# Optimization experiments

Measured on AMD Instinct MI355X. Metric: run time of the kernel, lower is better.

## Reference

```python
import jax, jax.numpy as jnp
import numpy as np

B = 128        # graphs per batch
N = 512        # nodes per graph (equal-size graphs -> dense mask all True)
F_IN = 128     # dataset.num_features
HID = 128      # hidden
C3 = 3 * HID   # num_layers * hidden (pool in_channels)
HEADS = 5
NC = 2         # num_classes
KC = NC + 1    # num_clusters2 = num_clusters_per_class*(num_classes+1) = 3
NC1 = NC       # num_clusters1 = num_clusters_per_class*num_classes = 2
OUT = 16       # pool out_channels
EPER = 8192    # edges per graph
TAU = 1.0
L1, L2 = 10.0, 0.01
BN_EPS = 1e-5


def setup_inputs() -> dict:
    key = jax.random.key(0)
    ks = jax.random.split(key, 12)
    Nn = B * N
    E = B * EPER
    x = jax.random.normal(ks[0], (Nn, F_IN), jnp.float32)
    local = jax.random.randint(ks[1], (2, E), 0, N)
    off = (jnp.repeat(jnp.arange(B), EPER) * N)[None, :]
    edge_index = (local + off).astype(jnp.int64)  # global node ids, per-graph blocks
    y = jax.random.randint(ks[2], (B,), 0, NC).astype(jnp.int64)

    def w(k_, shp, fan):
        return (jax.random.normal(k_, shp, jnp.float32) / np.sqrt(fan)).astype(jnp.float32)

    params = dict(
        W1=w(ks[3], (F_IN, HID), F_IN), b1=jnp.zeros((HID,), jnp.float32),
        W2=w(ks[4], (HID, HID), HID), b2=jnp.zeros((HID,), jnp.float32),
        W3=w(ks[5], (HID, HID), HID), b3=jnp.zeros((HID,), jnp.float32),
        bn_gamma=jnp.ones((C3,), jnp.float32), bn_beta=jnp.zeros((C3,), jnp.float32),
        k=w(ks[6], (HEADS, KC, C3), C3),
        lin_pool_W=w(ks[7], (C3, OUT), C3),
        lin1_W=w(ks[8], (NC1 * OUT, HID), NC1 * OUT), lin1_b=jnp.zeros((HID,), jnp.float32),
        lin2_W=w(ks[9], (HID, NC), HID), lin2_b=jnp.zeros((NC,), jnp.float32),
    )
    return dict(x=x, edge_index=edge_index, y=y, **params)


def reference(x, edge_index, y, W1, b1, W2, b2, W3, b3, bn_gamma, bn_beta, k,
              lin_pool_W, lin1_W, lin1_b, lin2_W, lin2_b):
    src, dst = edge_index[0], edge_index[1]
    Nn = x.shape[0]

    # GCNConv (normalize=False): out[dst] += (h @ W)[src] ; + bias
    def gcn(h, W, b):
        m = h @ W
        return jnp.zeros_like(m).at[dst].add(m[src]) + b

    h1 = jax.nn.relu(gcn(x, W1, b1))
    h2 = jax.nn.relu(gcn(h1, W2, b2))
    h3 = jax.nn.relu(gcn(h2, W3, b3))
    X = jnp.concatenate([h1, h2, h3], axis=1)  # [Nn, C3]

    # BatchNorm1d (training-mode batch stats, biased var)
    mu = X.mean(0)
    var = X.var(0)
    Xn = (X - mu) / jnp.sqrt(var + BN_EPS) * bn_gamma + bn_beta

    # --- IMPO pool ---
    H, K, C = k.shape
    k2 = k.reshape(H * K, C)
    # squared euclidean cdist: [H*K, Nn]
    d2 = jnp.maximum((k2 ** 2).sum(-1)[:, None] + (Xn ** 2).sum(-1)[None, :]
                     - 2.0 * (k2 @ Xn.T), 0.0)
    dist = (1.0 + d2 / TAU) ** (-(TAU + 1.0) / 2.0)
    dist = dist.reshape(H, K, B, N).transpose(2, 0, 3, 1)  # [B,H,N,K]
    Sh = dist / dist.sum(-1, keepdims=True)
    S = Sh.sum(1)  # sum over heads -> [B,N,K]; mask is all-True

    # per-graph adjacency aggregation: out[row] += S[col], then degree norm
    Sf = S.reshape(Nn, K)
    Sagg = jnp.zeros_like(Sf).at[src].add(Sf[dst])
    deg = (jnp.zeros((Nn,), Sf.dtype).at[src].add(1.0).at[dst].add(1.0)) / 2.0
    deg = jnp.where(deg == 0, 1.0, deg)
    S_raw = (Sagg / deg[:, None]).reshape(B, N, K)

    # use_gumbel=False path: softmax + hard argmax mask
    g = jax.nn.softmax(S_raw, axis=-1)
    onehot = jax.nn.one_hot(jnp.argmax(g, -1), K, dtype=g.dtype)
    Sfin = g * onehot

    xd = Xn.reshape(B, N, C)
    xp = jnp.einsum('bnk,bnc->bkc', Sfin, xd) @ lin_pool_W  # [B,K,OUT]
    out_x = xp[:, :NC1, :]

    # --- impo_loss ---
    yb = jnp.broadcast_to(y[:, None], (B, N))
    assigned = jnp.argmax(Sfin, -1)
    ac = assigned  # cluster_map is identity for num_clusters_per_class=1
    mr = (ac < NC) & (ac == yb)
    mw = (ac < NC) & (ac != yb)
    sum_loss = Sfin.sum(1)[:, :NC1].sum(1).mean()
    mf = (mr | mw).astype(Sfin.dtype)
    counts = jnp.zeros((NC,), Sfin.dtype).at[yb.reshape(-1)].add(mf.reshape(-1))
    bc = jnp.ones((NC,), Sfin.dtype) + counts
    weight = bc.max() / (bc + 0.001)
    logits = Sfin[..., :KC - 1]  # drop last cluster column
    logp = jax.nn.log_softmax(logits, axis=-1)
    ce = -jnp.take_along_axis(logp, yb[..., None], axis=-1)[..., 0]
    wsamp = weight[yb] * mf
    cel = (wsamp * ce).sum() / jnp.maximum(wsamp.sum(), 1e-12)
    total_loss = L1 * cel + L2 * sum_loss

    # head
    xf = out_x.reshape(B, -1)
    xf = jax.nn.relu(xf @ lin1_W + lin1_b)
    out = jax.nn.log_softmax(xf @ lin2_W + lin2_b, axis=-1)
    return (out, total_loss)
```

## Files before the change

### kernel.cpp

```cpp
#include <hip/hip_runtime.h>
#include <hip/hip_bf16.h>

#define BB 128
#define NV 512
#define NN (BB*NV)
#define EPER_C 8192
#define E_TOT (BB*EPER_C)
#define BN_EPS_F 1e-5f

typedef unsigned int u32;
typedef unsigned short u16;

__device__ __forceinline__ float bfu2f_lo(u32 w) { return __uint_as_float(w << 16); }
__device__ __forceinline__ float bfu2f_hi(u32 w) { return __uint_as_float(w & 0xFFFF0000u); }
__device__ __forceinline__ u16 f2bf(float f) {
    u32 u = __float_as_uint(f);
    u32 r = (u + 0x7FFFu + ((u >> 16) & 1u)) >> 16;
    return (u16)r;
}
__device__ __forceinline__ u32 pack2(float a, float b) {
    return (u32)f2bf(a) | ((u32)f2bf(b) << 16);
}
__device__ __forceinline__ float f16u2f(u16 h) {
    const u32 s = ((u32)h & 0x8000u) << 16;
    const u32 e = (h >> 10) & 0x1Fu;
    const u32 m = h & 0x3FFu;
    if (e == 0u) {
        float v = (float)m * 5.9604644775390625e-8f;
        return s ? -v : v;
    }
    if (e == 31u) return __uint_as_float(s | 0x7F800000u | (m << 13));
    return __uint_as_float(s | ((e + 112u) << 23) | (m << 13));
}
__device__ __forceinline__ float san(float v) {
    if (!(v == v)) return 0.f;
    return fminf(fmaxf(v, -1e30f), 1e30f);
}

__device__ __forceinline__ float2 h_ld2(const u32* H, size_t i2, int hf32) {
    float2 v;
    if (hf32) {
        v = ((const float2*)H)[i2];
    } else {
        const u32 w = H[i2];
        v.x = bfu2f_lo(w);
        v.y = bfu2f_hi(w);
    }
    return v;
}
__device__ __forceinline__ void h_st2(u32* H, size_t i2, float a, float b, int hf32) {
    if (hf32) {
        float2 v;
        v.x = a;
        v.y = b;
        ((float2*)H)[i2] = v;
    } else {
        H[i2] = pack2(a, b);
    }
}
__device__ __forceinline__ float h_ld1(const u32* H, size_t i, int hf32) {
    if (hf32) return ((const float*)H)[i];
    return __uint_as_float(((u32)((const u16*)H)[i]) << 16);
}

__global__ void fill_out_kernel(float* o, float v) {
    int i = blockIdx.x * 256 + threadIdx.x;
    if (i < 257) o[i] = v;
}

__global__ void init_kernel(u32* p, int n) {
    int i = blockIdx.x * 256 + threadIdx.x;
    if (i < n) p[i] = 0u;
}

__global__ void probe_kernel(const u32* g, const u32* e, u32* flags) {
    const int t = threadIdx.x;
    u32 acc = 0u;
    for (int i = t; i < 2048; i += 64) acc |= e[2 * i + 1];
#pragma unroll
    for (int s = 32; s > 0; s >>= 1) acc |= (u32)__shfl_xor((int)acc, s);
    if (t == 0) {
        const u32 w = g[0];
        u32 cls = 0u;
        if (w == 0x3F800000u) cls = 1u;
        else if (w == 0x3C003C00u) cls = 2u;
        flags[9] = cls;
        flags[8] = (acc != 0u) ? 1u : 0u;
    }
}

__device__ __forceinline__ int ld_src(const int* e, int is64, size_t i) {
    return (is64 ? e[2 * i] : e[i]) & (NN - 1);
}
__device__ __forceinline__ int ld_dst(const int* e, int is64, size_t i) {
    return (is64 ? e[2 * ((size_t)E_TOT + i)] : e[(size_t)E_TOT + i]) & (NN - 1);
}
__device__ __forceinline__ int ld_y(const int* y, int is64, int bi) {
    return (is64 ? y[2 * bi] : y[bi]) & 1;
}

#define CVT_TOT 66690
struct CvtPtrs { const void* p[14]; };
__global__ __launch_bounds__(256) void cvt_all_kernel(CvtPtrs ptrs, float* __restrict__ dst,
                                                      const u32* __restrict__ flags) {
    const int i = blockIdx.x * 256 + threadIdx.x;
    if (i >= CVT_TOT) return;
    const int kPof[14] = {0, 16384, 16512, 32896, 33024, 49408, 49536, 49920,
                          50304, 56064, 62208, 66304, 66432, 66688};
    const void* pp = ptrs.p[0];
    int base = 0;
#pragma unroll
    for (int s2 = 1; s2 < 14; ++s2) {
        if (i >= kPof[s2]) { pp = ptrs.p[s2]; base = kPof[s2]; }
    }
    const int off = i - base;
    const u32 cls = flags[9];
    float v;
    if (cls == 1u) v = ((const float*)pp)[off];
    else if (cls == 2u) v = f16u2f(((const u16*)pp)[off]);
    else v = __uint_as_float(((u32)((const u16*)pp)[off]) << 16);
    dst[i] = v;
}

__global__ __launch_bounds__(256) void csr_kernel(const int* __restrict__ eidx,
                                                  const u32* __restrict__ flags,
                                                  u16* __restrict__ sortedD,
                                                  u32* __restrict__ rpD) {
    __shared__ u32 cntD[512];
    __shared__ u32 offD[512];
    __shared__ u32 p[256];
    const int bi = blockIdx.x;
    const int t = threadIdx.x;
    const int is64 = (flags[8] == 0u);
    for (int i = t; i < 512; i += 256) cntD[i] = 0u;
    __syncthreads();
    const size_t eb = (size_t)bi * EPER_C;
    for (int e = t; e < EPER_C; e += 256) {
        const int dl = ld_dst(eidx, is64, eb + e) & 511;
        atomicAdd(&cntD[dl], 1u);
    }
    __syncthreads();
    const u32 a0 = cntD[2 * t], a1 = cntD[2 * t + 1];
    p[t] = a0 + a1;
    __syncthreads();
    for (int d = 1; d < 256; d <<= 1) {
        u32 va = p[t];
        if (t >= d) va += p[t - d];
        __syncthreads();
        p[t] = va;
        __syncthreads();
    }
    {
        const u32 exD = p[t] - (a0 + a1);
        offD[2 * t] = exD;
        offD[2 * t + 1] = exD + a0;
    }
    __syncthreads();
    for (int i = t; i < 512; i += 256) rpD[bi * 513 + i] = offD[i];
    if (t == 0) rpD[bi * 513 + 512] = EPER_C;
    for (int i = t; i < 512; i += 256) cntD[i] = 0u;
    __syncthreads();
    for (int e = t; e < EPER_C; e += 256) {
        const int sl = ld_src(eidx, is64, eb + e) & 511;
        const int dl = ld_dst(eidx, is64, eb + e) & 511;
        const u32 pos = offD[dl] + atomicAdd(&cntD[dl], 1u);
        sortedD[eb + pos] = (u16)sl;
    }
}

__global__ __launch_bounds__(1024, 4) void gemm_k(const u32* __restrict__ X2,
                                                  const float* __restrict__ Wc,
                                                  u32* __restrict__ Y2,
                                                  const u32* __restrict__ flags,
                                                  int xmode, int hf32) {
    __shared__ float xsT[128][132];
    __shared__ float ws[128][128];
    const int n0 = blockIdx.x * 128;
    const int t = threadIdx.x;
    const int tx = t & 31, ty = t >> 5;
    u32 cls;
    if (xmode) cls = flags[9];
    else cls = hf32 ? 1u : 0u;

    if (cls == 1u) {
        const float4* Xf4 = (const float4*)X2;
#pragma unroll
        for (int i = 0; i < 2; ++i) {
            const int idx = t + i * 1024;
            const int r = idx >> 4, q = idx & 15;
            const float4 v = Xf4[(size_t)(n0 + r) * 32 + q];
            xsT[4 * q + 0][r] = v.x;
            xsT[4 * q + 1][r] = v.y;
            xsT[4 * q + 2][r] = v.z;
            xsT[4 * q + 3][r] = v.w;
        }
    } else if (cls == 2u) {
#pragma unroll
        for (int i = 0; i < 4; ++i) {
            const int idx = t + i * 1024;
            const int r = idx >> 5, wq = idx & 31;
            const u32 w = X2[(size_t)(n0 + r) * 64 + wq];
            xsT[2 * wq + 0][r] = f16u2f((u16)(w & 0xFFFFu));
            xsT[2 * wq + 1][r] = f16u2f((u16)(w >> 16));
        }
    } else {
#pragma unroll
        for (int i = 0; i < 4; ++i) {
            const int idx = t + i * 1024;
            const int r = idx >> 5, wq = idx & 31;
            const u32 w = X2[(size_t)(n0 + r) * 64 + wq];
            xsT[2 * wq + 0][r] = bfu2f_lo(w);
            xsT[2 * wq + 1][r] = bfu2f_hi(w);
        }
    }
    {
        const float4* Wf4 = (const float4*)Wc;
#pragma unroll
        for (int i = 0; i < 2; ++i) {
            const int idx = t + i * 1024;
            const int kr = idx >> 5, cq = idx & 31;
            *(float4*)&ws[kr][4 * cq] = Wf4[(size_t)kr * 32 + cq];
        }
    }
    __syncthreads();

    float4 px0, px1, pw0, pw1;
    u32 pxu0 = 0, pxu1 = 0, pxu2 = 0, pxu3 = 0;
    if (cls == 1u) {
        const float4* Xf4 = (const float4*)X2;
        {
            const int r = t >> 4, q = t & 15;
            px0 = Xf4[(size_t)(n0 + r) * 32 + 16 + q];
        }
        {
            const int idx = t + 1024;
            const int r = idx >> 4, q = idx & 15;
            px1 = Xf4[(size_t)(n0 + r) * 32 + 16 + q];
        }
    } else {
        const int r0 = t >> 5, wq = t & 31;
        pxu0 = X2[(size_t)(n0 + r0) * 64 + 32 + wq];
        pxu1 = X2[(size_t)(n0 + r0 + 32) * 64 + 32 + wq];
        pxu2 = X2[(size_t)(n0 + r0 + 64) * 64 + 32 + wq];
        pxu3 = X2[(size_t)(n0 + r0 + 96) * 64 + 32 + wq];
    }
    {
        const float4* Wf4 = (const float4*)Wc;
        pw0 = Wf4[(size_t)(64 + (t >> 5)) * 32 + (t & 31)];
        pw1 = Wf4[(size_t)(96 + (t >> 5)) * 32 + (t & 31)];
    }

    float a[4][4];
#pragma unroll
    for (int r = 0; r < 4; ++r)
#pragma unroll
        for (int c = 0; c < 4; ++c) a[r][c] = 0.f;

#pragma unroll 4
    for (int k = 0; k < 64; ++k) {
        const float4 xv = *(const float4*)&xsT[k][4 * ty];
        const float4 wv = *(const float4*)&ws[k][4 * tx];
        a[0][0] += xv.x * wv.x; a[0][1] += xv.x * wv.y; a[0][2] += xv.x * wv.z; a[0][3] += xv.x * wv.w;
        a[1][0] += xv.y * wv.x; a[1][1] += xv.y * wv.y; a[1][2] += xv.y * wv.z; a[1][3] += xv.y * wv.w;
        a[2][0] += xv.z * wv.x; a[2][1] += xv.z * wv.y; a[2][2] += xv.z * wv.z; a[2][3] += xv.z * wv.w;
        a[3][0] += xv.w * wv.x; a[3][1] += xv.w * wv.y; a[3][2] += xv.w * wv.z; a[3][3] += xv.w * wv.w;
    }

    if (cls == 1u) {
        {
            const int r = t >> 4, q = t & 15;
            xsT[64 + 4 * q + 0][r] = px0.x;
            xsT[64 + 4 * q + 1][r] = px0.y;
            xsT[64 + 4 * q + 2][r] = px0.z;
            xsT[64 + 4 * q + 3][r] = px0.w;
        }
        {
            const int idx = t + 1024;
            const int r = idx >> 4, q = idx & 15;
            xsT[64 + 4 * q + 0][r] = px1.x;
            xsT[64 + 4 * q + 1][r] = px1.y;
            xsT[64 + 4 * q + 2][r] = px1.z;
            xsT[64 + 4 * q + 3][r] = px1.w;
        }
    } else if (cls == 2u) {
        const int r0 = t >> 5, wq = t & 31;
        xsT[64 + 2 * wq + 0][r0] = f16u2f((u16)(pxu0 & 0xFFFFu));
        xsT[64 + 2 * wq + 1][r0] = f16u2f((u16)(pxu0 >> 16));
        xsT[64 + 2 * wq + 0][r0 + 32] = f16u2f((u16)(pxu1 & 0xFFFFu));
        xsT[64 + 2 * wq + 1][r0 + 32] = f16u2f((u16)(pxu1 >> 16));
        xsT[64 + 2 * wq + 0][r0 + 64] = f16u2f((u16)(pxu2 & 0xFFFFu));
        xsT[64 + 2 * wq + 1][r0 + 64] = f16u2f((u16)(pxu2 >> 16));
        xsT[64 + 2 * wq + 0][r0 + 96] = f16u2f((u16)(pxu3 & 0xFFFFu));
        xsT[64 + 2 * wq + 1][r0 + 96] = f16u2f((u16)(pxu3 >> 16));
    } else {
        const int r0 = t >> 5, wq = t & 31;
        xsT[64 + 2 * wq + 0][r0] = bfu2f_lo(pxu0);
        xsT[64 + 2 * wq + 1][r0] = bfu2f_hi(pxu0);
        xsT[64 + 2 * wq + 0][r0 + 32] = bfu2f_lo(pxu1);
        xsT[64 + 2 * wq + 1][r0 + 32] = bfu2f_hi(pxu1);
        xsT[64 + 2 * wq + 0][r0 + 64] = bfu2f_lo(pxu2);
        xsT[64 + 2 * wq + 1][r0 + 64] = bfu2f_hi(pxu2);
        xsT[64 + 2 * wq + 0][r0 + 96] = bfu2f_lo(pxu3);
        xsT[64 + 2 * wq + 1][r0 + 96] = bfu2f_hi(pxu3);
    }
    {
        *(float4*)&ws[64 + (t >> 5)][4 * (t & 31)] = pw0;
        *(float4*)&ws[96 + (t >> 5)][4 * (t & 31)] = pw1;
    }
    __syncthreads();

#pragma unroll 4
    for (int k = 64; k < 128; ++k) {
        const float4 xv = *(const float4*)&xsT[k][4 * ty];
        const float4 wv = *(const float4*)&ws[k][4 * tx];
        a[0][0] += xv.x * wv.x; a[0][1] += xv.x * wv.y; a[0][2] += xv.x * wv.z; a[0][3] += xv.x * wv.w;
        a[1][0] += xv.y * wv.x; a[1][1] += xv.y * wv.y; a[1][2] += xv.y * wv.z; a[1][3] += xv.y * wv.w;
        a[2][0] += xv.z * wv.x; a[2][1] += xv.z * wv.y; a[2][2] += xv.z * wv.z; a[2][3] += xv.z * wv.w;
        a[3][0] += xv.w * wv.x; a[3][1] += xv.w * wv.y; a[3][2] += xv.w * wv.z; a[3][3] += xv.w * wv.w;
    }

#pragma unroll
    for (int r = 0; r < 4; ++r) {
        const size_t n = (size_t)n0 + 4 * ty + r;
        if (hf32) {
            float4 o;
            o.x = a[r][0]; o.y = a[r][1]; o.z = a[r][2]; o.w = a[r][3];
            ((float4*)Y2)[n * 32 + tx] = o;
        } else {
            Y2[n * 64 + 2 * tx + 0] = pack2(a[r][0], a[r][1]);
            Y2[n * 64 + 2 * tx + 1] = pack2(a[r][2], a[r][3]);
        }
    }
}

__global__ __launch_bounds__(1024) void gcn_lds_k(const u16* __restrict__ sortedD,
                                                  const u32* __restrict__ rpD,
                                                  const float* __restrict__ bias,
                                                  u32* __restrict__ M2,
                                                  float* __restrict__ bnacc,
                                                  int col_base, int hf32) {
    __shared__ float Ms[512 * 64];
    __shared__ u32 srt32[EPER_C / 2];
    __shared__ u32 rp[513];
    const int t = threadIdx.x;
    const int bi = blockIdx.x >> 1;
    const int hf = blockIdx.x & 1;
    const size_t rowbase = (size_t)bi * 512;
    const u16* srt = (const u16*)srt32;

    const u32* srcw = (const u32*)(sortedD + (size_t)bi * EPER_C);
    for (int i = t; i < EPER_C / 2; i += 1024) srt32[i] = srcw[i];
    for (int i = t; i < 513; i += 1024) rp[i] = rpD[bi * 513 + i];

    if (hf32) {
        const float4* src4 = (const float4*)M2;
        float4* dst4 = (float4*)Ms;
        for (int idx = t; idx < 512 * 16; idx += 1024) {
            const int r = idx >> 4, q = idx & 15;
            dst4[r * 16 + q] = src4[(rowbase + r) * 32 + hf * 16 + q];
        }
    } else {
        for (int idx = t; idx < 512 * 32; idx += 1024) {
            const int r = idx >> 5, q = idx & 31;
            const u32 w = M2[(rowbase + r) * 64 + hf * 32 + q];
            Ms[r * 64 + 2 * q] = bfu2f_lo(w);
            Ms[r * 64 + 2 * q + 1] = bfu2f_hi(w);
        }
    }
    __syncthreads();

    const int j = t & 15;
    const int g = t >> 4;
    const float4* M4 = (const float4*)Ms;
    const float bx = bias[hf * 64 + j * 4 + 0];
    const float by = bias[hf * 64 + j * 4 + 1];
    const float bz = bias[hf * 64 + j * 4 + 2];
    const float bw = bias[hf * 64 + j * 4 + 3];
    float S0 = 0.f, S1 = 0.f, S2 = 0.f, S3 = 0.f;
    float Q0 = 0.f, Q1 = 0.f, Q2 = 0.f, Q3 = 0.f;

#pragma unroll
    for (int gi = 0; gi < 8; ++gi) {
        const int l = g + gi * 64;
        u32 r1 = rp[l + 1];
        if (r1 > EPER_C) r1 = EPER_C;
        u32 r0 = rp[l];
        if (r0 > r1) r0 = r1;
        float ax = 0.f, ay = 0.f, az = 0.f, aw = 0.f;
        u32 idx = r0;
        for (; idx + 4 <= r1; idx += 4) {
            const int sa = srt[idx];
            const int sb = srt[idx + 1];
            const int sc = srt[idx + 2];
            const int sd = srt[idx + 3];
            const float4 va = M4[sa * 16 + j];
            const float4 vb = M4[sb * 16 + j];
            const float4 vc = M4[sc * 16 + j];
            const float4 vd = M4[sd * 16 + j];
            ax += va.x + vb.x; ay += va.y + vb.y; az += va.z + vb.z; aw += va.w + vb.w;
            ax += vc.x + vd.x; ay += vc.y + vd.y; az += vc.z + vd.z; aw += vc.w + vd.w;
        }
        for (; idx < r1; ++idx) {
            const int sa = srt[idx];
            const float4 va = M4[sa * 16 + j];
            ax += va.x; ay += va.y; az += va.z; aw += va.w;
        }
        float vx = san(ax + bx); vx = vx > 0.f ? vx : 0.f;
        float vy = san(ay + by); vy = vy > 0.f ? vy : 0.f;
        float vz = san(az + bz); vz = vz > 0.f ? vz : 0.f;
        float vw = san(aw + bw); vw = vw > 0.f ? vw : 0.f;
        if (hf32) {
            float4 o; o.x = vx; o.y = vy; o.z = vz; o.w = vw;
            ((float4*)M2)[(rowbase + l) * 32 + hf * 16 + j] = o;
        } else {
            const size_t pr = (rowbase + l) * 64 + hf * 32 + 2 * j;
            M2[pr] = pack2(vx, vy);
            M2[pr + 1] = pack2(vz, vw);
        }
        S0 += vx; S1 += vy; S2 += vz; S3 += vw;
        Q0 += vx * vx; Q1 += vy * vy; Q2 += vz * vz; Q3 += vw * vw;
    }

    S0 += __shfl_xor(S0, 16); Q0 += __shfl_xor(Q0, 16);
    S1 += __shfl_xor(S1, 16); Q1 += __shfl_xor(Q1, 16);
    S2 += __shfl_xor(S2, 16); Q2 += __shfl_xor(Q2, 16);
    S3 += __shfl_xor(S3, 16); Q3 += __shfl_xor(Q3, 16);
    S0 += __shfl_xor(S0, 32); Q0 += __shfl_xor(Q0, 32);
    S1 += __shfl_xor(S1, 32); Q1 += __shfl_xor(Q1, 32);
    S2 += __shfl_xor(S2, 32); Q2 += __shfl_xor(Q2, 32);
    S3 += __shfl_xor(S3, 32); Q3 += __shfl_xor(Q3, 32);

    __syncthreads();
    float* red = (float*)srt32;
    const int lane = t & 63;
    const int wid = t >> 6;
    if (lane < 16) {
        float* rw = &red[(wid * 16 + j) * 8];
        rw[0] = S0; rw[1] = Q0; rw[2] = S1; rw[3] = Q1;
        rw[4] = S2; rw[5] = Q2; rw[6] = S3; rw[7] = Q3;
    }
    __syncthreads();
    if (t < 128) {
        float s = 0.f;
        for (int w = 0; w < 16; ++w) s += red[w * 128 + t];
        const int jj = t >> 3;
        const int cc = (t >> 1) & 3;
        const int st = t & 1;
        atomicAdd(&bnacc[(size_t)(col_base + hf * 64 + jj * 4 + cc) * 2 + st], s);
    }
}

__global__ __launch_bounds__(384) void bn2_kernel(const float* __restrict__ bnacc,
                                                  const float* __restrict__ gamma,
                                                  const float* __restrict__ beta,
                                                  float* __restrict__ scaleA,
                                                  float* __restrict__ shiftA) {
    const int c = threadIdx.x;
    const float s = bnacc[c * 2 + 0];
    const float s2 = bnacc[c * 2 + 1];
    const float inv_n = 1.f / (float)NN;
    const float mu = san(s * inv_n);
    float var = san(s2 * inv_n - mu * mu);
    var = var > 0.f ? var : 0.f;
    const float sc = san(gamma[c] / sqrtf(var + BN_EPS_F));
    scaleA[c] = sc;
    shiftA[c] = san(beta[c] - mu * sc);
}

__global__ __launch_bounds__(256) void dist_kernel(const u32* __restrict__ h1,
                                                   const u32* __restrict__ h2,
                                                   const u32* __restrict__ h3,
                                                   const float* __restrict__ kc,
                                                   const float* __restrict__ scaleA,
                                                   const float* __restrict__ shiftA,
                                                   float4* __restrict__ Sf4, int hf32) {
    __shared__ float k2f[15 * 384];
    __shared__ float scl[384], shf[384];
    __shared__ float ksq[15];
    const int t = threadIdx.x;
    for (int i = t; i < 15 * 384; i += 256) k2f[i] = kc[i];
    for (int i = t; i < 384; i += 256) {
        scl[i] = scaleA[i];
        shf[i] = shiftA[i];
    }
    __syncthreads();
    if (t < 15) {
        float q = 0.f;
        for (int c2 = 0; c2 < 384; ++c2) {
            const float v = k2f[t * 384 + c2];
            q += v * v;
        }
        ksq[t] = q;
    }
    __syncthreads();
    const int n = blockIdx.x * 128 + (t >> 1);
    const int sub = t & 1;
    float acc[15];
#pragma unroll
    for (int j = 0; j < 15; ++j) acc[j] = 0.f;
    float xq = 0.f;
#pragma unroll
    for (int pL = 0; pL < 3; ++pL) {
        const u32* hp = (pL == 0) ? h1 : (pL == 1) ? h2 : h3;
        for (int q8 = sub; q8 < 16; q8 += 2) {
            float xv[8];
            if (hf32) {
                const float4 va = ((const float4*)hp)[(size_t)n * 32 + q8 * 2 + 0];
                const float4 vb = ((const float4*)hp)[(size_t)n * 32 + q8 * 2 + 1];
                xv[0] = va.x; xv[1] = va.y; xv[2] = va.z; xv[3] = va.w;
                xv[4] = vb.x; xv[5] = vb.y; xv[6] = vb.z; xv[7] = vb.w;
            } else {
                const uint4 w = ((const uint4*)hp)[(size_t)n * 16 + q8];
                xv[0] = bfu2f_lo(w.x); xv[1] = bfu2f_hi(w.x);
                xv[2] = bfu2f_lo(w.y); xv[3] = bfu2f_hi(w.y);
                xv[4] = bfu2f_lo(w.z); xv[5] = bfu2f_hi(w.z);
                xv[6] = bfu2f_lo(w.w); xv[7] = bfu2f_hi(w.w);
            }
            const int c = pL * 128 + q8 * 8;
#pragma unroll
            for (int i = 0; i < 8; ++i) {
                const float x = xv[i] * scl[c + i] + shf[c + i];
                xv[i] = x;
                xq += x * x;
            }
#pragma unroll
            for (int j = 0; j < 15; ++j) {
                const float* kr = &k2f[j * 384 + c];
                float a = acc[j];
#pragma unroll
                for (int i = 0; i < 8; ++i) a += xv[i] * kr[i];
                acc[j] = a;
            }
        }
    }
#pragma unroll
    for (int j = 0; j < 15; ++j) acc[j] += __shfl_xor(acc[j], 1);
    xq += __shfl_xor(xq, 1);
    if (sub == 0) {
        float dist[15];
#pragma unroll
        for (int j = 0; j < 15; ++j) {
            float d2 = san(ksq[j] + xq - 2.f * acc[j]);
            d2 = d2 > 0.f ? d2 : 0.f;
            dist[j] = 1.f / (1.f + d2);
        }
        float S0 = 0.f, S1 = 0.f, S2 = 0.f;
#pragma unroll
        for (int h = 0; h < 5; ++h) {
            const float a = dist[h * 3 + 0], b = dist[h * 3 + 1], cd = dist[h * 3 + 2];
            const float inv = 1.f / fmaxf(a + b + cd, 1e-30f);
            S0 += a * inv;
            S1 += b * inv;
            S2 += cd * inv;
        }
        float4 o;
        o.x = san(S0); o.y = san(S1); o.z = san(S2); o.w = 0.f;
        Sf4[n] = o;
    }
}

__global__ __launch_bounds__(256) void sagg_kernel(const int* __restrict__ eidx,
                                                   const u32* __restrict__ flags,
                                                   const float4* __restrict__ Sf4,
                                                   const int* __restrict__ y,
                                                   int* __restrict__ nodeK,
                                                   float* __restrict__ nodeW,
                                                   float* __restrict__ scal) {
    __shared__ float sacc[512 * 3];
    __shared__ unsigned int degc[512];
    __shared__ float rA[256], rB[256];
    const int bi = blockIdx.x;
    const int t = threadIdx.x;
    const int is64 = (flags[8] == 0u);
    for (int i = t; i < 512 * 3; i += 256) sacc[i] = 0.f;
    for (int i = t; i < 512; i += 256) degc[i] = 0u;
    __syncthreads();
    const size_t eb = (size_t)bi * EPER_C;
    for (int e = t; e < EPER_C; e += 256) {
        const int sg = ld_src(eidx, is64, eb + e);
        const int dg = ld_dst(eidx, is64, eb + e);
        const int sl = sg & 511;
        const int dl = dg & 511;
        const float4 sv = Sf4[dg];
        atomicAdd(&sacc[sl * 3 + 0], sv.x);
        atomicAdd(&sacc[sl * 3 + 1], sv.y);
        atomicAdd(&sacc[sl * 3 + 2], sv.z);
        atomicAdd(&degc[sl], 1u);
        atomicAdd(&degc[dl], 1u);
    }
    __syncthreads();
    float mfAcc = 0.f, slAcc = 0.f;
    for (int l = t; l < 512; l += 256) {
        const float cnt = (float)degc[l];
        const float degf = cnt > 0.f ? cnt * 0.5f : 1.f;
        const float inv = 1.f / degf;
        const float r0 = san(sacc[l * 3 + 0] * inv);
        const float r1 = san(sacc[l * 3 + 1] * inv);
        const float r2 = san(sacc[l * 3 + 2] * inv);
        int am = 0;
        float mx = r0;
        if (r1 > mx) { mx = r1; am = 1; }
        if (r2 > mx) { mx = r2; am = 2; }
        const float e0 = expf(r0 - mx), e1 = expf(r1 - mx), e2 = expf(r2 - mx);
        const float g = san(1.f / (e0 + e1 + e2));
        const int n = bi * 512 + l;
        nodeK[n] = am;
        nodeW[n] = g;
        if (am < 2) {
            mfAcc += 1.f;
            slAcc += g;
        }
    }
    rA[t] = mfAcc;
    rB[t] = slAcc;
    __syncthreads();
    for (int sft = 128; sft > 0; sft >>= 1) {
        if (t < sft) {
            rA[t] += rA[t + sft];
            rB[t] += rB[t + sft];
        }
        __syncthreads();
    }
    if (t == 0) {
        atomicAdd(&scal[ld_y(y, is64, bi)], rA[0]);
        atomicAdd(&scal[2], rB[0]);
    }
}

__global__ __launch_bounds__(256) void ce_kernel(const int* __restrict__ nodeK,
                                                 const float* __restrict__ nodeW,
                                                 const u32* __restrict__ flags,
                                                 const int* __restrict__ y,
                                                 float* __restrict__ scal) {
    const int n = blockIdx.x * 256 + threadIdx.x;
    const int bi = n >> 9;
    const int is64 = (flags[8] == 0u);
    const int kn = nodeK[n];
    float wce = 0.f, wsum = 0.f;
    if (kn >= 0 && kn < 2) {
        const float w = nodeW[n];
        const int yb = ld_y(y, is64, bi);
        const float l0 = (kn == 0) ? w : 0.f;
        const float l1 = (kn == 1) ? w : 0.f;
        const float m = fmaxf(l0, l1);
        const float lz = m + logf(expf(l0 - m) + expf(l1 - m));
        const float ce = lz - ((yb == 0) ? l0 : l1);
        const float bc0 = 1.f + scal[0];
        const float bc1 = 1.f + scal[1];
        const float bmax = fmaxf(bc0, bc1);
        const float wt = bmax / (((yb == 0) ? bc0 : bc1) + 0.001f);
        wce = san(wt * ce);
        wsum = san(wt);
    }
    __shared__ float rA[256], rB[256];
    const int t = threadIdx.x;
    rA[t] = wce;
    rB[t] = wsum;
    __syncthreads();
    for (int sft = 128; sft > 0; sft >>= 1) {
        if (t < sft) {
            rA[t] += rA[t + sft];
            rB[t] += rB[t + sft];
        }
        __syncthreads();
    }
    if (t == 0) {
        atomicAdd(&scal[3], rA[0]);
        atomicAdd(&scal[4], rB[0]);
    }
}

__global__ __launch_bounds__(384) void xp_kernel(const u32* __restrict__ h1,
                                                 const u32* __restrict__ h2,
                                                 const u32* __restrict__ h3,
                                                 const float* __restrict__ scaleA,
                                                 const float* __restrict__ shiftA,
                                                 const int* __restrict__ nodeK,
                                                 const float* __restrict__ nodeW,
                                                 float* __restrict__ xp, int hf32) {
    const int bi = blockIdx.x >> 2;
    const int ch = blockIdx.x & 3;
    const int c = threadIdx.x;
    const u32* harr = (c < 128) ? h1 : (c < 256) ? h2 : h3;
    const int cc = c & 127;
    const float sc = scaleA[c], sh = shiftA[c];
    float a0 = 0.f, a1 = 0.f;
    const int nb = bi * 512 + ch * 128;
    for (int l = 0; l < 128; ++l) {
        const int kn = nodeK[nb + l];
        if (kn >= 0 && kn < 2) {
            const float w = nodeW[nb + l];
            const float xv = h_ld1(harr, (size_t)(nb + l) * 128 + cc, hf32) * sc + sh;
            if (kn == 0) a0 += w * xv; else a1 += w * xv;
        }
    }
    atomicAdd(&xp[((size_t)bi * 2 + 0) * 384 + c], san(a0));
    atomicAdd(&xp[((size_t)bi * 2 + 1) * 384 + c], san(a1));
}

__global__ __launch_bounds__(128) void head_kernel(const float* __restrict__ xp,
                                                   const float* __restrict__ lpW,
                                                   const float* __restrict__ l1W,
                                                   const float* __restrict__ l1b,
                                                   const float* __restrict__ l2W,
                                                   const float* __restrict__ l2b,
                                                   float* __restrict__ outp) {
    const int bi = blockIdx.x;
    const int t = threadIdx.x;
    __shared__ float xfl[32];
    __shared__ float hidl[128];
    if (t < 32) {
        const int kk = t >> 4, o = t & 15;
        const float* xr = xp + ((size_t)bi * 2 + kk) * 384;
        float acc = 0.f;
        for (int c2 = 0; c2 < 384; ++c2) acc += xr[c2] * lpW[c2 * 16 + o];
        xfl[t] = san(acc);
    }
    __syncthreads();
    float acc = l1b[t];
    for (int i = 0; i < 32; ++i) acc += xfl[i] * l1W[i * 128 + t];
    hidl[t] = fmaxf(san(acc), 0.f);
    __syncthreads();
    if (t == 0) {
        float L0 = l2b[0], L1v = l2b[1];
        for (int j = 0; j < 128; ++j) {
            const float h = hidl[j];
            L0 += h * l2W[j * 2 + 0];
            L1v += h * l2W[j * 2 + 1];
        }
        L0 = san(L0); L1v = san(L1v);
        const float m = fmaxf(L0, L1v);
        const float ls = m + logf(expf(L0 - m) + expf(L1v - m));
        outp[bi * 2 + 0] = san(L0 - ls);
        outp[bi * 2 + 1] = san(L1v - ls);
    }
}

__global__ void fin_kernel(const float* __restrict__ scal, float* __restrict__ outp) {
    const float cel = san(scal[3] / fmaxf(scal[4], 1e-12f));
    const float total = san(10.f * cel + 0.01f * (scal[2] / (float)BB));
    outp[BB * 2] = total;
}

extern "C" void kernel_launch(void* const* d_in, const int* in_sizes, int n_in,
                              void* d_out, int out_size, void* d_ws, size_t ws_size,
                              hipStream_t stream) {
    (void)in_sizes; (void)n_in; (void)out_size;
    float* outp = (float*)d_out;

    const size_t tailW = (size_t)NN * 4 + (size_t)NN + (size_t)NN + 98304 + 16 + 768 + 768
                       + 66690 + 128 * 513 + (size_t)E_TOT / 2;
    const size_t needF = 3ull * NN * 128ull * 4ull + tailW * 4ull;
    const size_t needB = 3ull * NN * 128ull * 2ull + tailW * 4ull;
    int hf32;
    if (ws_size >= needF) hf32 = 1;
    else if (ws_size >= needB) hf32 = 0;
    else {
        fill_out_kernel<<<2, 256, 0, stream>>>(outp, 2000.f + (float)(ws_size >> 20));
        return;
    }

    const u32* xw = (const u32*)d_in[0];
    const int* eidx = (const int*)d_in[1];
    const int* y = (const int*)d_in[2];

    const size_t esz = hf32 ? 4u : 2u;
    char* base = (char*)d_ws;
    u32* H1 = (u32*)base;
    u32* H2 = (u32*)(base + (size_t)NN * 128 * esz);
    u32* H3 = (u32*)(base + 2 * (size_t)NN * 128 * esz);
    float* fb = (float*)(base + 3 * (size_t)NN * 128 * esz);
    float4* Sf4 = (float4*)fb;
    float* nodeW = fb + (size_t)NN * 4;
    int* nodeK = (int*)(nodeW + NN);
    float* xp = (float*)(nodeK + NN);
    float* scal = xp + 98304;
    u32* flags = (u32*)scal;
    float* bnacc = scal + 16;
    float* scaleA = bnacc + 768;
    float* shiftA = scaleA + 384;
    float* canon = shiftA + 384;
    u32* rpD = (u32*)(canon + 66690);
    u16* sortedD = (u16*)(rpD + 128 * 513);

    init_kernel<<<388, 256, 0, stream>>>((u32*)xp, 98304 + 16 + 768);
    probe_kernel<<<1, 64, 0, stream>>>((const u32*)d_in[9], (const u32*)eidx, flags);
    csr_kernel<<<BB, 256, 0, stream>>>(eidx, flags, sortedD, rpD);

    CvtPtrs cp;
    for (int i = 0; i < 14; ++i) cp.p[i] = d_in[3 + i];
    cvt_all_kernel<<<(CVT_TOT + 255) / 256, 256, 0, stream>>>(cp, canon, flags);

    gemm_k<<<NN / 128, 1024, 0, stream>>>(xw, canon + 0, H1, flags, 1, hf32);
    gcn_lds_k<<<BB * 2, 1024, 0, stream>>>(sortedD, rpD, canon + 16384, H1, bnacc, 0, hf32);
    gemm_k<<<NN / 128, 1024, 0, stream>>>(H1, canon + 16512, H2, flags, 0, hf32);
    gcn_lds_k<<<BB * 2, 1024, 0, stream>>>(sortedD, rpD, canon + 32896, H2, bnacc, 128, hf32);
    gemm_k<<<NN / 128, 1024, 0, stream>>>(H2, canon + 33024, H3, flags, 0, hf32);
    gcn_lds_k<<<BB * 2, 1024, 0, stream>>>(sortedD, rpD, canon + 49408, H3, bnacc, 256, hf32);
    bn2_kernel<<<1, 384, 0, stream>>>(bnacc, canon + 49536, canon + 49920, scaleA, shiftA);
    dist_kernel<<<NN / 128, 256, 0, stream>>>(H1, H2, H3, canon + 50304, scaleA, shiftA,
                                              Sf4, hf32);
    sagg_kernel<<<BB, 256, 0, stream>>>(eidx, flags, Sf4, y, nodeK, nodeW, scal);
    ce_kernel<<<NN / 256, 256, 0, stream>>>(nodeK, nodeW, flags, y, scal);
    xp_kernel<<<BB * 4, 384, 0, stream>>>(H1, H2, H3, scaleA, shiftA, nodeK, nodeW, xp, hf32);
    head_kernel<<<BB, 128, 0, stream>>>(xp, canon + 56064, canon + 62208, canon + 66304,
                                        canon + 66432, canon + 66688, outp);
    fin_kernel<<<1, 1, 0, stream>>>(scal, outp);
}
```

Baseline: 471.3 us.

## Restructure GEMM to 256 threads with 8x8 register tiles and double-buffered K chunks

Rewrites the node-feature GEMM kernel. Each block now uses 256 threads, each computing an 8x8 output micro-tile instead of 4x4, which raises arithmetic intensity per LDS read. The K dimension is split into four 32-wide chunks that are double-buffered in shared memory, with global loads for the next chunk issued before computing the current one. This shrinks LDS use and overlaps loads with FMAs, at the cost of more registers per thread and lower thread-level parallelism per block.

```diff
diff --git a/kernel.cpp b/kernel.cpp
--- a/kernel.cpp
+++ b/kernel.cpp
@@ -31,6 +31,10 @@
     }
     if (e == 31u) return __uint_as_float(s | 0x7F800000u | (m << 13));
     return __uint_as_float(s | ((e + 112u) << 23) | (m << 13));
+}
+__device__ __forceinline__ void u32tof2(u32 w, u32 cls, float& f0, float& f1) {
+    if (cls == 2u) { f0 = f16u2f((u16)(w & 0xFFFFu)); f1 = f16u2f((u16)(w >> 16)); }
+    else { f0 = bfu2f_lo(w); f1 = bfu2f_hi(w); }
 }
 __device__ __forceinline__ float san(float v) {
     if (!(v == v)) return 0.f;
@@ -168,167 +172,166 @@
     }
 }
 
-__global__ __launch_bounds__(1024, 4) void gemm_k(const u32* __restrict__ X2,
-                                                  const float* __restrict__ Wc,
-                                                  u32* __restrict__ Y2,
-                                                  const u32* __restrict__ flags,
-                                                  int xmode, int hf32) {
-    __shared__ float xsT[128][132];
-    __shared__ float ws[128][128];
+__global__ __launch_bounds__(256, 2) void gemm_k(const u32* __restrict__ X2,
+                                                 const float* __restrict__ Wc,
+                                                 u32* __restrict__ Y2,
+                                                 const u32* __restrict__ flags,
+                                                 int xmode, int hf32) {
+    __shared__ float xsT[2][32][132];
+    __shared__ float ws[2][32][128];
     const int n0 = blockIdx.x * 128;
     const int t = threadIdx.x;
-    const int tx = t & 31, ty = t >> 5;
+    const int tx = t & 15, ty = t >> 4;
     u32 cls;
     if (xmode) cls = flags[9];
     else cls = hf32 ? 1u : 0u;
 
-    if (cls == 1u) {
-        const float4* Xf4 = (const float4*)X2;
-#pragma unroll
-        for (int i = 0; i < 2; ++i) {
-            const int idx = t + i * 1024;
-            const int r = idx >> 4, q = idx & 15;
-            const float4 v = Xf4[(size_t)(n0 + r) * 32 + q];
-            xsT[4 * q + 0][r] = v.x;
-            xsT[4 * q + 1][r] = v.y;
-            xsT[4 * q + 2][r] = v.z;
-            xsT[4 * q + 3][r] = v.w;
-        }
-    } else if (cls == 2u) {
-#pragma unroll
-        for (int i = 0; i < 4; ++i) {
-            const int idx = t + i * 1024;
-            const int r = idx >> 5, wq = idx & 31;
-            const u32 w = X2[(size_t)(n0 + r) * 64 + wq];
-            xsT[2 * wq + 0][r] = f16u2f((u16)(w & 0xFFFFu));
-            xsT[2 * wq + 1][r] = f16u2f((u16)(w >> 16));
-        }
-    } else {
-#pragma unroll
-        for (int i = 0; i < 4; ++i) {
-            const int idx = t + i * 1024;
-            const int r = idx >> 5, wq = idx & 31;
-            const u32 w = X2[(size_t)(n0 + r) * 64 + wq];
-            xsT[2 * wq + 0][r] = bfu2f_lo(w);
-            xsT[2 * wq + 1][r] = bfu2f_hi(w);
-        }
-    }
-    {
-        const float4* Wf4 = (const float4*)Wc;
-#pragma unroll
-        for (int i = 0; i < 2; ++i) {
-            const int idx = t + i * 1024;
-            const int kr = idx >> 5, cq = idx & 31;
-            *(float4*)&ws[kr][4 * cq] = Wf4[(size_t)kr * 32 + cq];
-        }
-    }
-    __syncthreads();
-
-    float4 px0, px1, pw0, pw1;
-    u32 pxu0 = 0, pxu1 = 0, pxu2 = 0, pxu3 = 0;
-    if (cls == 1u) {
-        const float4* Xf4 = (const float4*)X2;
-        {
-            const int r = t >> 4, q = t & 15;
-            px0 = Xf4[(size_t)(n0 + r) * 32 + 16 + q];
-        }
-        {
-            const int idx = t + 1024;
-            const int r = idx >> 4, q = idx & 15;
-            px1 = Xf4[(size_t)(n0 + r) * 32 + 16 + q];
-        }
-    } else {
-        const int r0 = t >> 5, wq = t & 31;
-        pxu0 = X2[(size_t)(n0 + r0) * 64 + 32 + wq];
-        pxu1 = X2[(size_t)(n0 + r0 + 32) * 64 + 32 + wq];
-        pxu2 = X2[(size_t)(n0 + r0 + 64) * 64 + 32 + wq];
-        pxu3 = X2[(size_t)(n0 + r0 + 96) * 64 + 32 + wq];
-    }
-    {
-        const float4* Wf4 = (const float4*)Wc;
-        pw0 = Wf4[(size_t)(64 + (t >> 5)) * 32 + (t & 31)];
-        pw1 = Wf4[(size_t)(96 + (t >> 5)) * 32 + (t & 31)];
-    }
-
-    float a[4][4];
-#pragma unroll
-    for (int r = 0; r < 4; ++r)
-#pragma unroll
-        for (int c = 0; c < 4; ++c) a[r][c] = 0.f;
-
-#pragma unroll 4
-    for (int k = 0; k < 64; ++k) {
-        const float4 xv = *(const float4*)&xsT[k][4 * ty];
-        const float4 wv = *(const float4*)&ws[k][4 * tx];
-        a[0][0] += xv.x * wv.x; a[0][1] += xv.x * wv.y; a[0][2] += xv.x * wv.z; a[0][3] += xv.x * wv.w;
-        a[1][0] += xv.y * wv.x; a[1][1] += xv.y * wv.y; a[1][2] += xv.y * wv.z; a[1][3] += xv.y * wv.w;
-        a[2][0] += xv.z * wv.x; a[2][1] += xv.z * wv.y; a[2][2] += xv.z * wv.z; a[2][3] += xv.z * wv.w;
-        a[3][0] += xv.w * wv.x; a[3][1] += xv.w * wv.y; a[3][2] += xv.w * wv.z; a[3][3] += xv.w * wv.w;
-    }
-
-    if (cls == 1u) {
-        {
-            const int r = t >> 4, q = t & 15;
-            xsT[64 + 4 * q + 0][r] = px0.x;
-            xsT[64 + 4 * q + 1][r] = px0.y;
-            xsT[64 + 4 * q + 2][r] = px0.z;
-            xsT[64 + 4 * q + 3][r] = px0.w;
-        }
-        {
-            const int idx = t + 1024;
-            const int r = idx >> 4, q = idx & 15;
-            xsT[64 + 4 * q + 0][r] = px1.x;
-            xsT[64 + 4 * q + 1][r] = px1.y;
-            xsT[64 + 4 * q + 2][r] = px1.z;
-            xsT[64 + 4 * q + 3][r] = px1.w;
-        }
-    } else if (cls == 2u) {
-        const int r0 = t >> 5, wq = t & 31;
-        xsT[64 + 2 * wq + 0][r0] = f16u2f((u16)(pxu0 & 0xFFFFu));
-        xsT[64 + 2 * wq + 1][r0] = f16u2f((u16)(pxu0 >> 16));
-        xsT[64 + 2 * wq + 0][r0 + 32] = f16u2f((u16)(pxu1 & 0xFFFFu));
-        xsT[64 + 2 * wq + 1][r0 + 32] = f16u2f((u16)(pxu1 >> 16));
-        xsT[64 + 2 * wq + 0][r0 + 64] = f16u2f((u16)(pxu2 & 0xFFFFu));
-        xsT[64 + 2 * wq + 1][r0 + 64] = f16u2f((u16)(pxu2 >> 16));
-        xsT[64 + 2 * wq + 0][r0 + 96] = f16u2f((u16)(pxu3 & 0xFFFFu));
-        xsT[64 + 2 * wq + 1][r0 + 96] = f16u2f((u16)(pxu3 >> 16));
-    } else {
-        const int r0 = t >> 5, wq = t & 31;
-        xsT[64 + 2 * wq + 0][r0] = bfu2f_lo(pxu0);
-        xsT[64 + 2 * wq + 1][r0] = bfu2f_hi(pxu0);
-        xsT[64 + 2 * wq + 0][r0 + 32] = bfu2f_lo(pxu1);
-        xsT[64 + 2 * wq + 1][r0 + 32] = bfu2f_hi(pxu1);
-        xsT[64 + 2 * wq + 0][r0 + 64] = bfu2f_lo(pxu2);
-        xsT[64 + 2 * wq + 1][r0 + 64] = bfu2f_hi(pxu2);
-        xsT[64 + 2 * wq + 0][r0 + 96] = bfu2f_lo(pxu3);
-        xsT[64 + 2 * wq + 1][r0 + 96] = bfu2f_hi(pxu3);
-    }
-    {
-        *(float4*)&ws[64 + (t >> 5)][4 * (t & 31)] = pw0;
-        *(float4*)&ws[96 + (t >> 5)][4 * (t & 31)] = pw1;
-    }
-    __syncthreads();
-
-#pragma unroll 4
-    for (int k = 64; k < 128; ++k) {
-        const float4 xv = *(const float4*)&xsT[k][4 * ty];
-        const float4 wv = *(const float4*)&ws[k][4 * tx];
-        a[0][0] += xv.x * wv.x; a[0][1] += xv.x * wv.y; a[0][2] += xv.x * wv.z; a[0][3] += xv.x * wv.w;
-        a[1][0] += xv.y * wv.x; a[1][1] += xv.y * wv.y; a[1][2] += xv.y * wv.z; a[1][3] += xv.y * wv.w;
-        a[2][0] += xv.z * wv.x; a[2][1] += xv.z * wv.y; a[2][2] += xv.z * wv.z; a[2][3] += xv.z * wv.w;
-        a[3][0] += xv.w * wv.x; a[3][1] += xv.w * wv.y; a[3][2] += xv.w * wv.z; a[3][3] += xv.w * wv.w;
-    }
-
-#pragma unroll
-    for (int r = 0; r < 4; ++r) {
-        const size_t n = (size_t)n0 + 4 * ty + r;
-        if (hf32) {
-            float4 o;
-            o.x = a[r][0]; o.y = a[r][1]; o.z = a[r][2]; o.w = a[r][3];
-            ((float4*)Y2)[n * 32 + tx] = o;
-        } else {
-            Y2[n * 64 + 2 * tx + 0] = pack2(a[r][0], a[r][1]);
-            Y2[n * 64 + 2 * tx + 1] = pack2(a[r][2], a[r][3]);
+    float4 px[4];
+    uint4 pxu[2];
+    float4 pw[4];
+
+#define GLOADX(kc) do { \
+    if (cls == 1u) { \
+        const float4* Xf4 = (const float4*)X2; \
+_Pragma("unroll") \
+        for (int i_ = 0; i_ < 4; ++i_) { \
+            const int task = t + i_ * 256; \
+            const int r_ = task >> 3, q_ = task & 7; \
+            px[i_] = Xf4[(size_t)(n0 + r_) * 32 + (kc) * 8 + q_]; \
+        } \
+    } else { \
+        const uint4* Xu4 = (const uint4*)X2; \
+_Pragma("unroll") \
+        for (int i_ = 0; i_ < 2; ++i_) { \
+            const int task = t + i_ * 256; \
+            const int r_ = task >> 2, uq_ = task & 3; \
+            pxu[i_] = Xu4[(size_t)(n0 + r_) * 16 + (kc) * 4 + uq_]; \
+        } \
+    } \
+} while (0)
+
+#define GLOADW(kc) do { \
+    const float4* Wf4 = (const float4*)Wc; \
+_Pragma("unroll") \
+    for (int i_ = 0; i_ < 4; ++i_) { \
+        const int task = t + i_ * 256; \
+        const int kr_ = task >> 5, cq_ = task & 31; \
+        pw[i_] = Wf4[(size_t)((kc) * 32 + kr_) * 32 + cq_]; \
+    } \
+} while (0)
+
+#define SWRITE(bi) do { \
+    if (cls == 1u) { \
+_Pragma("unroll") \
+        for (int i_ = 0; i_ < 4; ++i_) { \
+            const int task = t + i_ * 256; \
+            const int r_ = task >> 3, q_ = task & 7; \
+            xsT[bi][4 * q_ + 0][r_] = px[i_].x; \
+            xsT[bi][4 * q_ + 1][r_] = px[i_].y; \
+            xsT[bi][4 * q_ + 2][r_] = px[i_].z; \
+            xsT[bi][4 * q_ + 3][r_] = px[i_].w; \
+        } \
+    } else { \
+_Pragma("unroll") \
+        for (int i_ = 0; i_ < 2; ++i_) { \
+            const int task = t + i_ * 256; \
+            const int r_ = task >> 2, uq_ = task & 3; \
+            const u32* wp_ = (const u32*)&pxu[i_]; \
+_Pragma("unroll") \
+            for (int m_ = 0; m_ < 4; ++m_) { \
+                float f0_, f1_; \
+                u32tof2(wp_[m_], cls, f0_, f1_); \
+                xsT[bi][uq_ * 8 + 2 * m_ + 0][r_] = f0_; \
+                xsT[bi][uq_ * 8 + 2 * m_ + 1][r_] = f1_; \
+            } \
+        } \
+    } \
+_Pragma("unroll") \
+    for (int i_ = 0; i_ < 4; ++i_) { \
+        const int task = t + i_ * 256; \
+        const int kr_ = task >> 5, cq_ = task & 31; \
+        *(float4*)&ws[bi][kr_][4 * cq_] = pw[i_]; \
+    } \
+} while (0)
+
+    GLOADX(0);
+    GLOADW(0);
+    SWRITE(0);
+    __syncthreads();
+
+    float a[2][4][2][4];
+#pragma unroll
+    for (int rh = 0; rh < 2; ++rh)
+#pragma unroll
+        for (int j = 0; j < 4; ++j)
+#pragma unroll
+            for (int ch = 0; ch < 2; ++ch)
+#pragma unroll
+                for (int i = 0; i < 4; ++i) a[rh][j][ch][i] = 0.f;
+
+    for (int c = 0; c < 4; ++c) {
+        if (c < 3) {
+            GLOADX(c + 1);
+            GLOADW(c + 1);
+        }
+        const float (*xb)[132] = xsT[c & 1];
+        const float (*wb)[128] = ws[c & 1];
+#pragma unroll 8
+        for (int k = 0; k < 32; ++k) {
+            const float4 xa = *(const float4*)&xb[k][4 * ty];
+            const float4 xc = *(const float4*)&xb[k][64 + 4 * ty];
+            const float4 wa = *(const float4*)&wb[k][4 * tx];
+            const float4 wc = *(const float4*)&wb[k][64 + 4 * tx];
+            const float xr0[4] = {xa.x, xa.y, xa.z, xa.w};
+            const float xr1[4] = {xc.x, xc.y, xc.z, xc.w};
+#pragma unroll
+            for (int j = 0; j < 4; ++j) {
+                a[0][j][0][0] += xr0[j] * wa.x;
+                a[0][j][0][1] += xr0[j] * wa.y;
+                a[0][j][0][2] += xr0[j] * wa.z;
+                a[0][j][0][3] += xr0[j] * wa.w;
+                a[0][j][1][0] += xr0[j] * wc.x;
+                a[0][j][1][1] += xr0[j] * wc.y;
+                a[0][j][1][2] += xr0[j] * wc.z;
+                a[0][j][1][3] += xr0[j] * wc.w;
+                a[1][j][0][0] += xr1[j] * wa.x;
+                a[1][j][0][1] += xr1[j] * wa.y;
+                a[1][j][0][2] += xr1[j] * wa.z;
+                a[1][j][0][3] += xr1[j] * wa.w;
+                a[1][j][1][0] += xr1[j] * wc.x;
+                a[1][j][1][1] += xr1[j] * wc.y;
+                a[1][j][1][2] += xr1[j] * wc.z;
+                a[1][j][1][3] += xr1[j] * wc.w;
+            }
+        }
+        if (c < 3) {
+            SWRITE((c + 1) & 1);
+            __syncthreads();
+        }
+    }
+#undef GLOADX
+#undef GLOADW
+#undef SWRITE
+
+#pragma unroll
+    for (int rh = 0; rh < 2; ++rh) {
+#pragma unroll
+        for (int j = 0; j < 4; ++j) {
+            const size_t n = (size_t)n0 + rh * 64 + 4 * ty + j;
+#pragma unroll
+            for (int ch = 0; ch < 2; ++ch) {
+                if (hf32) {
+                    float4 o;
+                    o.x = a[rh][j][ch][0];
+                    o.y = a[rh][j][ch][1];
+                    o.z = a[rh][j][ch][2];
+                    o.w = a[rh][j][ch][3];
+                    ((float4*)Y2)[n * 32 + ch * 16 + tx] = o;
+                } else {
+                    Y2[n * 64 + ch * 32 + 2 * tx + 0] = pack2(a[rh][j][ch][0], a[rh][j][ch][1]);
+                    Y2[n * 64 + ch * 32 + 2 * tx + 1] = pack2(a[rh][j][ch][2], a[rh][j][ch][3]);
+                }
+            }
         }
     }
 }
@@ -791,11 +794,11 @@
     for (int i = 0; i < 14; ++i) cp.p[i] = d_in[3 + i];
     cvt_all_kernel<<<(CVT_TOT + 255) / 256, 256, 0, stream>>>(cp, canon, flags);
 
-    gemm_k<<<NN / 128, 1024, 0, stream>>>(xw, canon + 0, H1, flags, 1, hf32);
+    gemm_k<<<NN / 128, 256, 0, stream>>>(xw, canon + 0, H1, flags, 1, hf32);
     gcn_lds_k<<<BB * 2, 1024, 0, stream>>>(sortedD, rpD, canon + 16384, H1, bnacc, 0, hf32);
-    gemm_k<<<NN / 128, 1024, 0, stream>>>(H1, canon + 16512, H2, flags, 0, hf32);
+    gemm_k<<<NN / 128, 256, 0, stream>>>(H1, canon + 16512, H2, flags, 0, hf32);
     gcn_lds_k<<<BB * 2, 1024, 0, stream>>>(sortedD, rpD, canon + 32896, H2, bnacc, 128, hf32);
-    gemm_k<<<NN / 128, 1024, 0, stream>>>(H2, canon + 33024, H3, flags, 0, hf32);
+    gemm_k<<<NN / 128, 256, 0, stream>>>(H2, canon + 33024, H3, flags, 0, hf32);
     gcn_lds_k<<<BB * 2, 1024, 0, stream>>>(sortedD, rpD, canon + 49408, H3, bnacc, 256, hf32);
     bn2_kernel<<<1, 384, 0, stream>>>(bnacc, canon + 49536, canon + 49920, scaleA, shiftA);
     dist_kernel<<<NN / 128, 256, 0, stream>>>(H1, H2, H3, canon + 50304, scaleA, shiftA,
```

New measurement: 463.7 us. Within noise of the previous version (-1.6%).
